# Performance work log

Measured on AMD Instinct MI355X. Metric: run time of the kernel, lower is better.

The kernel has to match this reference:

```python
import jax, jax.numpy as jnp
import numpy as np
from jax import lax

CIN = 3
NUM_BINS = 9
EPS_MAG = 1e-6
EPS_IN = 1e-5  # torch InstanceNorm2d default eps


def setup_inputs() -> dict:
    key = jax.random.key(0)
    kx, = jax.random.split(key, 1)
    x = jax.random.normal(kx, (32, CIN, 512, 512), dtype=jnp.float32)
    # Sobel kernels, repeated across input channels exactly as in _init_weights
    sx = jnp.array([[-1.0, 0.0, 1.0], [-2.0, 0.0, 2.0], [-1.0, 0.0, 1.0]], jnp.float32)
    sy = jnp.array([[-1.0, -2.0, -1.0], [0.0, 0.0, 0.0], [1.0, 2.0, 1.0]], jnp.float32)
    sobel_x = jnp.broadcast_to(sx, (1, CIN, 3, 3)).astype(jnp.float32)  # OIHW
    sobel_y = jnp.broadcast_to(sy, (1, CIN, 3, 3)).astype(jnp.float32)
    # Orientation 1x1 conv weights: [num_bins, 2] = [cos(theta), sin(theta)]
    angles = jnp.linspace(0.0, np.pi, NUM_BINS + 1)[:-1]
    orient_w = jnp.stack([jnp.cos(angles), jnp.sin(angles)], axis=1).astype(jnp.float32)
    # InstanceNorm affine params (torch init: weight=1, bias=0)
    gamma = jnp.ones((NUM_BINS,), jnp.float32)
    beta = jnp.zeros((NUM_BINS,), jnp.float32)
    return {"x": x, "sobel_x": sobel_x, "sobel_y": sobel_y,
            "orient_w": orient_w, "gamma": gamma, "beta": beta}


def _conv3x3(x, w):
    # x: [B,C,H,W], w: [1,C,3,3] -> [B,1,H,W] (padding=1 == SAME)
    return lax.conv_general_dilated(
        x, w, window_strides=(1, 1), padding="SAME",
        dimension_numbers=("NCHW", "OIHW", "NCHW"))


def reference(x, sobel_x, sobel_y, orient_w, gamma, beta):
    # Gradient operator
    gx = _conv3x3(x, sobel_x)  # [B,1,H,W]
    gy = _conv3x3(x, sobel_y)  # [B,1,H,W]
    # Orientation binning
    mag = jnp.sqrt(gx * gx + gy * gy + EPS_MAG)  # [B,1,H,W]
    # 1x1 conv over channels [gx, gy] with weight [K,2] == wx*gx + wy*gy
    wx = orient_w[:, 0][None, :, None, None]
    wy = orient_w[:, 1][None, :, None, None]
    resp = gx * wx + gy * wy  # [B,K,H,W]
    weights = jax.nn.softmax(resp, axis=1)
    binned = mag * weights  # [B,K,H,W]
    # InstanceNorm2d(affine=True): per-(b,c) stats over HxW, biased variance
    mean = jnp.mean(binned, axis=(2, 3), keepdims=True)
    var = jnp.var(binned, axis=(2, 3), keepdims=True)
    xhat = (binned - mean) * lax.rsqrt(var + EPS_IN)
    return xhat * gamma[None, :, None, None] + beta[None, :, None, None]
```

## Files before the change

### kernel.cpp

```cpp
#include <hip/hip_runtime.h>
#include <cstdint>
#include <cstddef>

typedef float f4 __attribute__((ext_vector_type(4)));

constexpr int Bn  = 32;
constexpr int Cin = 3;
constexpr int Hh  = 512;
constexpr int Ww  = 512;
constexpr int Kb  = 9;
constexpr float EPS_MAG_F = 1e-6f;
constexpr float EPS_IN_F  = 1e-5f;

constexpr int TW = 128;
constexpr int TH = 32;
constexpr int LDS_W = TW + 8;
constexpr int LDS_H = TH + 2;
constexpr int BLOCKS_X = Ww / TW;
constexpr int BLOCKS_Y = Hh / TH;
constexpr int BLOCKS_PER_IMG = BLOCKS_X * BLOCKS_Y;
constexpr int NSLOT = LDS_H * (LDS_W / 4);

template <int PASS>
__global__ __launch_bounds__(256) void goe_tile_kernel(
    const float* __restrict__ x,
    const float* __restrict__ orient_w,
    const float2* __restrict__ stats,
    float* __restrict__ partial,
    float* __restrict__ out)
{
    __shared__ float sm[LDS_H][LDS_W];

    const int b  = blockIdx.z;
    const int h0 = blockIdx.y * TH;
    const int w0 = blockIdx.x * TW;
    const int tx = threadIdx.x;
    const int ty = threadIdx.y;
    const int tid = ty * 32 + tx;

    const size_t plane = (size_t)Hh * Ww;
    const float* xb = x + (size_t)b * Cin * plane;

#pragma unroll
    for (int it = 0; it < 5; ++it) {
        const int slot = tid + it * 256;
        if (slot < NSLOT) {
            const int row = slot / 34;
            const int q   = slot - row * 34;
            const int gh  = h0 - 1 + row;
            const int gw  = w0 - 4 + q * 4;
            f4 v = {0.f, 0.f, 0.f, 0.f};
            if ((unsigned)gh < (unsigned)Hh && (unsigned)gw < (unsigned)Ww) {
                const float* p = xb + (size_t)gh * Ww + gw;
                const f4 a = *(const f4*)(p);
                const f4 c = *(const f4*)(p + plane);
                const f4 d = *(const f4*)(p + 2 * plane);
                v = a + c + d;
            }
            *(f4*)&sm[row][q * 4] = v;
        }
    }

    float wx[Kb], wy[Kb];
#pragma unroll
    for (int k = 0; k < Kb; ++k) {
        wx[k] = orient_w[2 * k];
        wy[k] = orient_w[2 * k + 1];
    }

    float2 st[Kb];
    if (PASS == 1) {
#pragma unroll
        for (int k = 0; k < Kb; ++k) st[k] = stats[b * Kb + k];
    }

    float acc_s[Kb], acc_q[Kb];
    if (PASS == 0) {
#pragma unroll
        for (int k = 0; k < Kb; ++k) { acc_s[k] = 0.f; acc_q[k] = 0.f; }
    }

    __syncthreads();

    const int cb    = tx * 4;
    const int rbase = ty * 4;

    float A[6], Bf[6], Cf[6];

    auto load_row = [&](float (&R)[6], int sr) {
        R[0] = sm[sr][cb + 3];
        const f4 M = *(const f4*)&sm[sr][cb + 4];
        R[1] = M.x; R[2] = M.y; R[3] = M.z; R[4] = M.w;
        R[5] = sm[sr][cb + 8];
    };

    auto do_row = [&](const float (&T)[6], const float (&M)[6],
                      const float (&Bo)[6], int rr) {
        float ov[Kb][4];
#pragma unroll
        for (int j = 0; j < 4; ++j) {
            const float gx = (T[j + 2] - T[j]) + 2.f * (M[j + 2] - M[j]) +
                             (Bo[j + 2] - Bo[j]);
            const float gy = (Bo[j] + 2.f * Bo[j + 1] + Bo[j + 2]) -
                             (T[j] + 2.f * T[j + 1] + T[j + 2]);
            const float mag = sqrtf(fmaf(gx, gx, fmaf(gy, gy, EPS_MAG_F)));
            float e[Kb], se = 0.f;
#pragma unroll
            for (int k = 0; k < Kb; ++k) {
                e[k] = __expf(fmaf(gx, wx[k], fmaf(gy, wy[k], -mag)));
                se += e[k];
            }
            const float minv = __fdividef(mag, se);
#pragma unroll
            for (int k = 0; k < Kb; ++k) {
                const float bv = e[k] * minv;
                if (PASS == 0) {
                    acc_s[k] += bv;
                    acc_q[k] = fmaf(bv, bv, acc_q[k]);
                } else {
                    ov[k][j] = fmaf(bv, st[k].x, st[k].y);
                }
            }
        }
        if (PASS == 1) {
            const size_t ob = ((size_t)(b * Kb) * Hh + (h0 + rbase + rr)) * Ww
                              + w0 + cb;
#pragma unroll
            for (int k = 0; k < Kb; ++k) {
                f4 v4 = {ov[k][0], ov[k][1], ov[k][2], ov[k][3]};
                __builtin_nontemporal_store(v4, (f4*)&out[ob + (size_t)k * plane]);
            }
        }
    };

    load_row(A,  rbase);
    load_row(Bf, rbase + 1);
    load_row(Cf, rbase + 2); do_row(A,  Bf, Cf, 0);
    load_row(A,  rbase + 3); do_row(Bf, Cf, A,  1);
    load_row(Bf, rbase + 4); do_row(Cf, A,  Bf, 2);
    load_row(Cf, rbase + 5); do_row(A,  Bf, Cf, 3);

    if (PASS == 0) {
#pragma unroll
        for (int k = 0; k < Kb; ++k) {
            for (int off = 32; off > 0; off >>= 1) {
                acc_s[k] += __shfl_down(acc_s[k], off);
                acc_q[k] += __shfl_down(acc_q[k], off);
            }
        }
        __syncthreads();
        float* red = &sm[0][0];
        const int wid = tid >> 6, lane = tid & 63;
        if (lane == 0) {
#pragma unroll
            for (int k = 0; k < Kb; ++k) {
                red[wid * 18 + k]     = acc_s[k];
                red[wid * 18 + 9 + k] = acc_q[k];
            }
        }
        __syncthreads();
        if (tid < 18) {
            const float v = red[tid] + red[18 + tid] + red[36 + tid] + red[54 + tid];
            const int blk = blockIdx.y * BLOCKS_X + blockIdx.x;
            partial[((size_t)b * BLOCKS_PER_IMG + blk) * 18 + tid] = v;
        }
    }
}

__global__ __launch_bounds__(64) void goe_stats_kernel(
    const float* __restrict__ partial,
    const float* __restrict__ gamma,
    const float* __restrict__ beta,
    float2* __restrict__ stats)
{
    const int idx = blockIdx.x;
    const int b = idx / Kb, k = idx % Kb;
    const int t = threadIdx.x;

    const float* p = partial + ((size_t)b * BLOCKS_PER_IMG + t) * 18;
    float s = p[k];
    float q = p[9 + k];
    for (int off = 32; off > 0; off >>= 1) {
        s += __shfl_down(s, off);
        q += __shfl_down(q, off);
    }
    if (t == 0) {
        const float invN = 1.f / (float)(Hh * Ww);
        const float mean = s * invN;
        const float var  = fmaxf(q * invN - mean * mean, 0.f);
        const float rstd = rsqrtf(var + EPS_IN_F);
        const float sc   = rstd * gamma[k];
        stats[idx] = make_float2(sc, beta[k] - mean * sc);
    }
}

extern "C" void kernel_launch(void* const* d_in, const int* in_sizes, int n_in,
                              void* d_out, int out_size, void* d_ws, size_t ws_size,
                              hipStream_t stream)
{
    const float* x        = (const float*)d_in[0];
    const float* orient_w = (const float*)d_in[3];
    const float* gamma    = (const float*)d_in[4];
    const float* beta     = (const float*)d_in[5];
    float* out = (float*)d_out;

    float*  partial = (float*)d_ws;
    float2* stats   = (float2*)((char*)d_ws +
                       (size_t)Bn * BLOCKS_PER_IMG * 18 * sizeof(float));

    const dim3 grid(BLOCKS_X, BLOCKS_Y, Bn);
    const dim3 block(32, 8);

    hipLaunchKernelGGL((goe_tile_kernel<0>), grid, block, 0, stream,
                       x, orient_w, nullptr, partial, nullptr);
    hipLaunchKernelGGL(goe_stats_kernel, dim3(Bn * Kb), dim3(64), 0, stream,
                       partial, gamma, beta, stats);
    hipLaunchKernelGGL((goe_tile_kernel<1>), grid, block, 0, stream,
                       x, orient_w, stats, nullptr, out);
}
```

Baseline: 116.8 us.

## Replace LDS tiles with per-wavefront row streaming and shuffle-based halos

Drops the shared-memory tile and block-level synchronisation. Each wavefront now streams an 8-row by 256-column strip, reading rows directly from global memory and taking horizontal neighbours with lane shuffles plus edge-lane loads. The exponential becomes exp2 with log2e pre-folded into the weights, and sqrt and reciprocal use hardware intrinsics. The price is a larger vertical halo: 10 rows loaded per 8 output rows instead of 34 per 32, twice the stats partials, and launch bounds that constrain register use.

```diff
diff --git a/kernel.cpp b/kernel.cpp
--- a/kernel.cpp
+++ b/kernel.cpp
@@ -5,67 +5,63 @@
 typedef float f4 __attribute__((ext_vector_type(4)));
 
 constexpr int Bn  = 32;
-constexpr int Cin = 3;
 constexpr int Hh  = 512;
 constexpr int Ww  = 512;
 constexpr int Kb  = 9;
 constexpr float EPS_MAG_F = 1e-6f;
 constexpr float EPS_IN_F  = 1e-5f;
-
-constexpr int TW = 128;
-constexpr int TH = 32;
-constexpr int LDS_W = TW + 8;
-constexpr int LDS_H = TH + 2;
-constexpr int BLOCKS_X = Ww / TW;
-constexpr int BLOCKS_Y = Hh / TH;
-constexpr int BLOCKS_PER_IMG = BLOCKS_X * BLOCKS_Y;
-constexpr int NSLOT = LDS_H * (LDS_W / 4);
+constexpr float LOG2E_F   = 1.4426950408889634f;
+
+constexpr int CH      = 8;
+constexpr int STRIPS  = 2;
+constexpr int CHUNKS  = Hh / CH;
+constexpr int WPI     = STRIPS * CHUNKS;
+constexpr int WAVES_TOTAL = Bn * WPI;
+constexpr int WPB     = 4;
+constexpr int NBLK    = WAVES_TOTAL / WPB;
+
+#if __has_builtin(__builtin_amdgcn_exp2f)
+#define EXP2F(x) __builtin_amdgcn_exp2f(x)
+#else
+#define EXP2F(x) exp2f(x)
+#endif
+#if __has_builtin(__builtin_amdgcn_sqrtf)
+#define SQRTF(x) __builtin_amdgcn_sqrtf(x)
+#else
+#define SQRTF(x) sqrtf(x)
+#endif
+#if __has_builtin(__builtin_amdgcn_rcpf)
+#define RCPF(x) __builtin_amdgcn_rcpf(x)
+#else
+#define RCPF(x) (1.0f / (x))
+#endif
 
 template <int PASS>
-__global__ __launch_bounds__(256) void goe_tile_kernel(
+__global__ __launch_bounds__(256, 4) void goe_stream_kernel(
     const float* __restrict__ x,
     const float* __restrict__ orient_w,
     const float2* __restrict__ stats,
     float* __restrict__ partial,
     float* __restrict__ out)
 {
-    __shared__ float sm[LDS_H][LDS_W];
-
-    const int b  = blockIdx.z;
-    const int h0 = blockIdx.y * TH;
-    const int w0 = blockIdx.x * TW;
-    const int tx = threadIdx.x;
-    const int ty = threadIdx.y;
-    const int tid = ty * 32 + tx;
+    const int lane = threadIdx.x;
+    const int wid  = blockIdx.x * WPB + threadIdx.y;
+    const int b     = wid >> 7;
+    const int rem   = wid & (WPI - 1);
+    const int strip = rem >> 6;
+    const int chunk = rem & (CHUNKS - 1);
+    const int r0    = chunk * CH;
+    const int c0    = strip * 256;
+    const int cl    = c0 + lane * 4;
 
     const size_t plane = (size_t)Hh * Ww;
-    const float* xb = x + (size_t)b * Cin * plane;
-
-#pragma unroll
-    for (int it = 0; it < 5; ++it) {
-        const int slot = tid + it * 256;
-        if (slot < NSLOT) {
-            const int row = slot / 34;
-            const int q   = slot - row * 34;
-            const int gh  = h0 - 1 + row;
-            const int gw  = w0 - 4 + q * 4;
-            f4 v = {0.f, 0.f, 0.f, 0.f};
-            if ((unsigned)gh < (unsigned)Hh && (unsigned)gw < (unsigned)Ww) {
-                const float* p = xb + (size_t)gh * Ww + gw;
-                const f4 a = *(const f4*)(p);
-                const f4 c = *(const f4*)(p + plane);
-                const f4 d = *(const f4*)(p + 2 * plane);
-                v = a + c + d;
-            }
-            *(f4*)&sm[row][q * 4] = v;
-        }
-    }
-
-    float wx[Kb], wy[Kb];
+    const float* xb = x + (size_t)b * 3 * plane;
+
+    float wx2[Kb], wy2[Kb];
 #pragma unroll
     for (int k = 0; k < Kb; ++k) {
-        wx[k] = orient_w[2 * k];
-        wy[k] = orient_w[2 * k + 1];
+        wx2[k] = orient_w[2 * k]     * LOG2E_F;
+        wy2[k] = orient_w[2 * k + 1] * LOG2E_F;
     }
 
     float2 st[Kb];
@@ -74,28 +70,40 @@
         for (int k = 0; k < Kb; ++k) st[k] = stats[b * Kb + k];
     }
 
-    float acc_s[Kb], acc_q[Kb];
+    float accs[Kb], accq[Kb];
     if (PASS == 0) {
 #pragma unroll
-        for (int k = 0; k < Kb; ++k) { acc_s[k] = 0.f; acc_q[k] = 0.f; }
-    }
-
-    __syncthreads();
-
-    const int cb    = tx * 4;
-    const int rbase = ty * 4;
-
-    float A[6], Bf[6], Cf[6];
-
-    auto load_row = [&](float (&R)[6], int sr) {
-        R[0] = sm[sr][cb + 3];
-        const f4 M = *(const f4*)&sm[sr][cb + 4];
-        R[1] = M.x; R[2] = M.y; R[3] = M.z; R[4] = M.w;
-        R[5] = sm[sr][cb + 8];
+        for (int k = 0; k < Kb; ++k) { accs[k] = 0.f; accq[k] = 0.f; }
+    }
+
+    const bool is_edge = (lane == 0) || (lane == 63);
+    const int  ecol    = (lane == 0) ? (c0 - 1) : (c0 + 256);
+    const bool ecol_ok = is_edge && ((unsigned)ecol < (unsigned)Ww);
+
+    auto load_row = [&](int r, float (&R6)[6]) {
+        f4 m = {0.f, 0.f, 0.f, 0.f};
+        const bool rok = (unsigned)r < (unsigned)Hh;
+        if (rok) {
+            const float* p = xb + (size_t)r * Ww + cl;
+            const f4 a = *(const f4*)(p);
+            const f4 c = *(const f4*)(p + plane);
+            const f4 d = *(const f4*)(p + 2 * plane);
+            m = a + c + d;
+        }
+        float ev = 0.f;
+        if (ecol_ok && rok) {
+            const float* q = xb + (size_t)r * Ww + ecol;
+            ev = q[0] + q[plane] + q[2 * plane];
+        }
+        float L  = __shfl_up(m.w, 1);
+        float Rr = __shfl_down(m.x, 1);
+        if (lane == 0)  L  = ev;
+        if (lane == 63) Rr = ev;
+        R6[0] = L; R6[1] = m.x; R6[2] = m.y; R6[3] = m.z; R6[4] = m.w; R6[5] = Rr;
     };
 
     auto do_row = [&](const float (&T)[6], const float (&M)[6],
-                      const float (&Bo)[6], int rr) {
+                      const float (&Bo)[6], int r) {
         float ov[Kb][4];
 #pragma unroll
         for (int j = 0; j < 4; ++j) {
@@ -103,28 +111,29 @@
                              (Bo[j + 2] - Bo[j]);
             const float gy = (Bo[j] + 2.f * Bo[j + 1] + Bo[j + 2]) -
                              (T[j] + 2.f * T[j + 1] + T[j + 2]);
-            const float mag = sqrtf(fmaf(gx, gx, fmaf(gy, gy, EPS_MAG_F)));
+            const float m2   = fmaf(gx, gx, fmaf(gy, gy, EPS_MAG_F));
+            const float mag  = SQRTF(m2);
+            const float mag2 = mag * LOG2E_F;
             float e[Kb], se = 0.f;
 #pragma unroll
             for (int k = 0; k < Kb; ++k) {
-                e[k] = __expf(fmaf(gx, wx[k], fmaf(gy, wy[k], -mag)));
+                e[k] = EXP2F(fmaf(gx, wx2[k], fmaf(gy, wy2[k], -mag2)));
                 se += e[k];
             }
-            const float minv = __fdividef(mag, se);
+            const float minv = mag * RCPF(se);
 #pragma unroll
             for (int k = 0; k < Kb; ++k) {
                 const float bv = e[k] * minv;
                 if (PASS == 0) {
-                    acc_s[k] += bv;
-                    acc_q[k] = fmaf(bv, bv, acc_q[k]);
+                    accs[k] += bv;
+                    accq[k] = fmaf(bv, bv, accq[k]);
                 } else {
                     ov[k][j] = fmaf(bv, st[k].x, st[k].y);
                 }
             }
         }
         if (PASS == 1) {
-            const size_t ob = ((size_t)(b * Kb) * Hh + (h0 + rbase + rr)) * Ww
-                              + w0 + cb;
+            const size_t ob = ((size_t)(b * Kb) * Hh + r) * Ww + cl;
 #pragma unroll
             for (int k = 0; k < Kb; ++k) {
                 f4 v4 = {ov[k][0], ov[k][1], ov[k][2], ov[k][3]};
@@ -133,36 +142,33 @@
         }
     };
 
-    load_row(A,  rbase);
-    load_row(Bf, rbase + 1);
-    load_row(Cf, rbase + 2); do_row(A,  Bf, Cf, 0);
-    load_row(A,  rbase + 3); do_row(Bf, Cf, A,  1);
-    load_row(Bf, rbase + 4); do_row(Cf, A,  Bf, 2);
-    load_row(Cf, rbase + 5); do_row(A,  Bf, Cf, 3);
+    float A[6], Bf[6], Cf[6];
+    load_row(r0 - 1, A);
+    load_row(r0,     Bf);
+    load_row(r0 + 1, Cf); do_row(A,  Bf, Cf, r0 + 0);
+    load_row(r0 + 2, A);  do_row(Bf, Cf, A,  r0 + 1);
+    load_row(r0 + 3, Bf); do_row(Cf, A,  Bf, r0 + 2);
+    load_row(r0 + 4, Cf); do_row(A,  Bf, Cf, r0 + 3);
+    load_row(r0 + 5, A);  do_row(Bf, Cf, A,  r0 + 4);
+    load_row(r0 + 6, Bf); do_row(Cf, A,  Bf, r0 + 5);
+    load_row(r0 + 7, Cf); do_row(A,  Bf, Cf, r0 + 6);
+    load_row(r0 + 8, A);  do_row(Bf, Cf, A,  r0 + 7);
 
     if (PASS == 0) {
 #pragma unroll
         for (int k = 0; k < Kb; ++k) {
             for (int off = 32; off > 0; off >>= 1) {
-                acc_s[k] += __shfl_down(acc_s[k], off);
-                acc_q[k] += __shfl_down(acc_q[k], off);
-            }
-        }
-        __syncthreads();
-        float* red = &sm[0][0];
-        const int wid = tid >> 6, lane = tid & 63;
+                accs[k] += __shfl_down(accs[k], off);
+                accq[k] += __shfl_down(accq[k], off);
+            }
+        }
         if (lane == 0) {
-#pragma unroll
-            for (int k = 0; k < Kb; ++k) {
-                red[wid * 18 + k]     = acc_s[k];
-                red[wid * 18 + 9 + k] = acc_q[k];
-            }
-        }
-        __syncthreads();
-        if (tid < 18) {
-            const float v = red[tid] + red[18 + tid] + red[36 + tid] + red[54 + tid];
-            const int blk = blockIdx.y * BLOCKS_X + blockIdx.x;
-            partial[((size_t)b * BLOCKS_PER_IMG + blk) * 18 + tid] = v;
+            float* p = partial + (size_t)wid * 18;
+#pragma unroll
+            for (int k = 0; k < Kb; ++k) {
+                p[k]     = accs[k];
+                p[9 + k] = accq[k];
+            }
         }
     }
 }
@@ -177,9 +183,10 @@
     const int b = idx / Kb, k = idx % Kb;
     const int t = threadIdx.x;
 
-    const float* p = partial + ((size_t)b * BLOCKS_PER_IMG + t) * 18;
-    float s = p[k];
-    float q = p[9 + k];
+    const float* p0 = partial + ((size_t)b * WPI + t) * 18;
+    const float* p1 = p0 + 64 * 18;
+    float s = p0[k]     + p1[k];
+    float q = p0[9 + k] + p1[9 + k];
     for (int off = 32; off > 0; off >>= 1) {
         s += __shfl_down(s, off);
         q += __shfl_down(q, off);
@@ -206,15 +213,15 @@
 
     float*  partial = (float*)d_ws;
     float2* stats   = (float2*)((char*)d_ws +
-                       (size_t)Bn * BLOCKS_PER_IMG * 18 * sizeof(float));
-
-    const dim3 grid(BLOCKS_X, BLOCKS_Y, Bn);
-    const dim3 block(32, 8);
-
-    hipLaunchKernelGGL((goe_tile_kernel<0>), grid, block, 0, stream,
+                       (size_t)WAVES_TOTAL * 18 * sizeof(float));
+
+    const dim3 grid(NBLK);
+    const dim3 block(64, WPB);
+
+    hipLaunchKernelGGL((goe_stream_kernel<0>), grid, block, 0, stream,
                        x, orient_w, nullptr, partial, nullptr);
     hipLaunchKernelGGL(goe_stats_kernel, dim3(Bn * Kb), dim3(64), 0, stream,
                        partial, gamma, beta, stats);
-    hipLaunchKernelGGL((goe_tile_kernel<1>), grid, block, 0, stream,
+    hipLaunchKernelGGL((goe_stream_kernel<1>), grid, block, 0, stream,
                        x, orient_w, stats, nullptr, out);
 }
```

After: 182.5 us. +56.2%, slower.

## Cache channel-summed input in workspace and use cheaper exp2/sqrt/rcp intrinsics

Applied to the files above, without the earlier changes.

Pass 0 writes the channel-summed image (one plane per batch) to workspace, and pass 1 reads that plane instead of re-reading all three input channels, so pass 1 reads a third as much input. The stencil now precomputes horizontal differences and sums per row and fetches neighbour columns with lane shuffles. The softmax uses exp2 with log2e folded into the weights, and the magnitude uses raw sqrt and reciprocal intrinsics. In exchange, pass 0 gains a 32 MB workspace write, and the raw intrinsics may lose some precision.

```diff
diff --git a/kernel.cpp b/kernel.cpp
--- a/kernel.cpp
+++ b/kernel.cpp
@@ -5,12 +5,12 @@
 typedef float f4 __attribute__((ext_vector_type(4)));
 
 constexpr int Bn  = 32;
-constexpr int Cin = 3;
 constexpr int Hh  = 512;
 constexpr int Ww  = 512;
 constexpr int Kb  = 9;
 constexpr float EPS_MAG_F = 1e-6f;
 constexpr float EPS_IN_F  = 1e-5f;
+constexpr float LOG2E_F   = 1.4426950408889634f;
 
 constexpr int TW = 128;
 constexpr int TH = 32;
@@ -21,9 +21,29 @@
 constexpr int BLOCKS_PER_IMG = BLOCKS_X * BLOCKS_Y;
 constexpr int NSLOT = LDS_H * (LDS_W / 4);
 
+#if __has_builtin(__builtin_amdgcn_exp2f)
+#define EXP2F(x) __builtin_amdgcn_exp2f(x)
+#else
+#define EXP2F(x) exp2f(x)
+#endif
+#if __has_builtin(__builtin_amdgcn_sqrtf)
+#define SQRTF(x) __builtin_amdgcn_sqrtf(x)
+#else
+#define SQRTF(x) sqrtf(x)
+#endif
+#if __has_builtin(__builtin_amdgcn_rcpf)
+#define RCPF(x) __builtin_amdgcn_rcpf(x)
+#else
+#define RCPF(x) (1.0f / (x))
+#endif
+
+struct RowW { float hd[4]; float hs[4]; };
+
 template <int PASS>
 __global__ __launch_bounds__(256) void goe_tile_kernel(
     const float* __restrict__ x,
+    const float* __restrict__ s_in,
+    float* __restrict__ s_out,
     const float* __restrict__ orient_w,
     const float2* __restrict__ stats,
     float* __restrict__ partial,
@@ -37,9 +57,10 @@
     const int tx = threadIdx.x;
     const int ty = threadIdx.y;
     const int tid = ty * 32 + tx;
+    const int lane = tid & 63;
 
     const size_t plane = (size_t)Hh * Ww;
-    const float* xb = x + (size_t)b * Cin * plane;
+    const float* xb = x + (size_t)b * 3 * plane;
 
 #pragma unroll
     for (int it = 0; it < 5; ++it) {
@@ -49,23 +70,32 @@
             const int q   = slot - row * 34;
             const int gh  = h0 - 1 + row;
             const int gw  = w0 - 4 + q * 4;
+            const bool ok = (unsigned)gh < (unsigned)Hh && (unsigned)gw < (unsigned)Ww;
             f4 v = {0.f, 0.f, 0.f, 0.f};
-            if ((unsigned)gh < (unsigned)Hh && (unsigned)gw < (unsigned)Ww) {
-                const float* p = xb + (size_t)gh * Ww + gw;
-                const f4 a = *(const f4*)(p);
-                const f4 c = *(const f4*)(p + plane);
-                const f4 d = *(const f4*)(p + 2 * plane);
-                v = a + c + d;
-            }
-            *(f4*)&sm[row][q * 4] = v;
-        }
-    }
-
-    float wx[Kb], wy[Kb];
+            if (PASS == 0) {
+                if (ok) {
+                    const float* p = xb + (size_t)gh * Ww + gw;
+                    const f4 a = *(const f4*)(p);
+                    const f4 c = *(const f4*)(p + plane);
+                    const f4 d = *(const f4*)(p + 2 * plane);
+                    v = a + c + d;
+                }
+                *(f4*)&sm[row][q * 4] = v;
+                if ((unsigned)(row - 1) < 32u && (unsigned)(q - 1) < 32u) {
+                    *(f4*)&s_out[((size_t)b * Hh + gh) * Ww + gw] = v;
+                }
+            } else {
+                if (ok) v = *(const f4*)&s_in[((size_t)b * Hh + gh) * Ww + gw];
+                *(f4*)&sm[row][q * 4] = v;
+            }
+        }
+    }
+
+    float wx2[Kb], wy2[Kb];
 #pragma unroll
     for (int k = 0; k < Kb; ++k) {
-        wx[k] = orient_w[2 * k];
-        wy[k] = orient_w[2 * k + 1];
+        wx2[k] = orient_w[2 * k]     * LOG2E_F;
+        wy2[k] = orient_w[2 * k + 1] * LOG2E_F;
     }
 
     float2 st[Kb];
@@ -74,10 +104,10 @@
         for (int k = 0; k < Kb; ++k) st[k] = stats[b * Kb + k];
     }
 
-    float acc_s[Kb], acc_q[Kb];
+    float accs[Kb], accq[Kb];
     if (PASS == 0) {
 #pragma unroll
-        for (int k = 0; k < Kb; ++k) { acc_s[k] = 0.f; acc_q[k] = 0.f; }
+        for (int k = 0; k < Kb; ++k) { accs[k] = 0.f; accq[k] = 0.f; }
     }
 
     __syncthreads();
@@ -85,38 +115,44 @@
     const int cb    = tx * 4;
     const int rbase = ty * 4;
 
-    float A[6], Bf[6], Cf[6];
-
-    auto load_row = [&](float (&R)[6], int sr) {
-        R[0] = sm[sr][cb + 3];
-        const f4 M = *(const f4*)&sm[sr][cb + 4];
-        R[1] = M.x; R[2] = M.y; R[3] = M.z; R[4] = M.w;
-        R[5] = sm[sr][cb + 8];
+    auto load_row = [&](int sr) -> RowW {
+        const f4 m = *(const f4*)&sm[sr][cb + 4];
+        float L  = __shfl_up(m.w, 1);
+        float Rr = __shfl_down(m.x, 1);
+        if ((lane & 31) == 0)  L  = sm[sr][cb + 3];
+        if ((lane & 31) == 31) Rr = sm[sr][cb + 8];
+        RowW r;
+        r.hd[0] = m.y - L;   r.hd[1] = m.z - m.x;
+        r.hd[2] = m.w - m.y; r.hd[3] = Rr - m.z;
+        r.hs[0] = fmaf(2.f, m.x, L + m.y);
+        r.hs[1] = fmaf(2.f, m.y, m.x + m.z);
+        r.hs[2] = fmaf(2.f, m.z, m.y + m.w);
+        r.hs[3] = fmaf(2.f, m.w, m.z + Rr);
+        return r;
     };
 
-    auto do_row = [&](const float (&T)[6], const float (&M)[6],
-                      const float (&Bo)[6], int rr) {
+    auto do_row = [&](const RowW& T, const RowW& M, const RowW& Bo, int rr) {
         float ov[Kb][4];
 #pragma unroll
         for (int j = 0; j < 4; ++j) {
-            const float gx = (T[j + 2] - T[j]) + 2.f * (M[j + 2] - M[j]) +
-                             (Bo[j + 2] - Bo[j]);
-            const float gy = (Bo[j] + 2.f * Bo[j + 1] + Bo[j + 2]) -
-                             (T[j] + 2.f * T[j + 1] + T[j + 2]);
-            const float mag = sqrtf(fmaf(gx, gx, fmaf(gy, gy, EPS_MAG_F)));
+            const float gx = fmaf(2.f, M.hd[j], T.hd[j] + Bo.hd[j]);
+            const float gy = Bo.hs[j] - T.hs[j];
+            const float m2   = fmaf(gx, gx, fmaf(gy, gy, EPS_MAG_F));
+            const float mag  = SQRTF(m2);
+            const float mag2 = mag * LOG2E_F;
             float e[Kb], se = 0.f;
 #pragma unroll
             for (int k = 0; k < Kb; ++k) {
-                e[k] = __expf(fmaf(gx, wx[k], fmaf(gy, wy[k], -mag)));
+                e[k] = EXP2F(fmaf(gx, wx2[k], fmaf(gy, wy2[k], -mag2)));
                 se += e[k];
             }
-            const float minv = __fdividef(mag, se);
+            const float minv = mag * RCPF(se);
 #pragma unroll
             for (int k = 0; k < Kb; ++k) {
                 const float bv = e[k] * minv;
                 if (PASS == 0) {
-                    acc_s[k] += bv;
-                    acc_q[k] = fmaf(bv, bv, acc_q[k]);
+                    accs[k] += bv;
+                    accq[k] = fmaf(bv, bv, accq[k]);
                 } else {
                     ov[k][j] = fmaf(bv, st[k].x, st[k].y);
                 }
@@ -133,29 +169,29 @@
         }
     };
 
-    load_row(A,  rbase);
-    load_row(Bf, rbase + 1);
-    load_row(Cf, rbase + 2); do_row(A,  Bf, Cf, 0);
-    load_row(A,  rbase + 3); do_row(Bf, Cf, A,  1);
-    load_row(Bf, rbase + 4); do_row(Cf, A,  Bf, 2);
-    load_row(Cf, rbase + 5); do_row(A,  Bf, Cf, 3);
+    RowW A  = load_row(rbase);
+    RowW Bf = load_row(rbase + 1);
+    RowW Cf = load_row(rbase + 2); do_row(A,  Bf, Cf, 0);
+    A  = load_row(rbase + 3);      do_row(Bf, Cf, A,  1);
+    Bf = load_row(rbase + 4);      do_row(Cf, A,  Bf, 2);
+    Cf = load_row(rbase + 5);      do_row(A,  Bf, Cf, 3);
 
     if (PASS == 0) {
 #pragma unroll
         for (int k = 0; k < Kb; ++k) {
             for (int off = 32; off > 0; off >>= 1) {
-                acc_s[k] += __shfl_down(acc_s[k], off);
-                acc_q[k] += __shfl_down(acc_q[k], off);
+                accs[k] += __shfl_down(accs[k], off);
+                accq[k] += __shfl_down(accq[k], off);
             }
         }
         __syncthreads();
         float* red = &sm[0][0];
-        const int wid = tid >> 6, lane = tid & 63;
-        if (lane == 0) {
-#pragma unroll
-            for (int k = 0; k < Kb; ++k) {
-                red[wid * 18 + k]     = acc_s[k];
-                red[wid * 18 + 9 + k] = acc_q[k];
+        const int wid = tid >> 6, ln = tid & 63;
+        if (ln == 0) {
+#pragma unroll
+            for (int k = 0; k < Kb; ++k) {
+                red[wid * 18 + k]     = accs[k];
+                red[wid * 18 + 9 + k] = accq[k];
             }
         }
         __syncthreads();
@@ -204,17 +240,18 @@
     const float* beta     = (const float*)d_in[5];
     float* out = (float*)d_out;
 
-    float*  partial = (float*)d_ws;
-    float2* stats   = (float2*)((char*)d_ws +
+    float*  s_ws    = (float*)d_ws;
+    float*  partial = (float*)((char*)d_ws + (size_t)Bn * Hh * Ww * sizeof(float));
+    float2* stats   = (float2*)((char*)partial +
                        (size_t)Bn * BLOCKS_PER_IMG * 18 * sizeof(float));
 
     const dim3 grid(BLOCKS_X, BLOCKS_Y, Bn);
     const dim3 block(32, 8);
 
     hipLaunchKernelGGL((goe_tile_kernel<0>), grid, block, 0, stream,
-                       x, orient_w, nullptr, partial, nullptr);
+                       x, nullptr, s_ws, orient_w, nullptr, partial, nullptr);
     hipLaunchKernelGGL(goe_stats_kernel, dim3(Bn * Kb), dim3(64), 0, stream,
                        partial, gamma, beta, stats);
     hipLaunchKernelGGL((goe_tile_kernel<1>), grid, block, 0, stream,
-                       x, orient_w, stats, nullptr, out);
+                       nullptr, s_ws, nullptr, orient_w, stats, nullptr, out);
 }
```

New measurement: 111.4 us. 4.7% less time.
